# Kernel tuning notes

Measured on AMD Instinct MI355X. Metric: run time of the kernel, lower is better.

## Reference

```python
import jax, jax.numpy as jnp
import numpy as np

HEAD_DIM = 128
ROPE_THETA = 500000.0  # Llama3
NEG_INF = -1e9


def _apply_rope(t, cos, sin):
    # t: [b, s, h, d]; cos/sin: [s, d//2]
    b, s, h, d = t.shape
    tr = t.reshape(b, s, h, d // 2, 2)
    xr, xi = tr[..., 0], tr[..., 1]
    c = cos[None, :, None, :]
    sn = sin[None, :, None, :]
    out = jnp.stack([xr * c - xi * sn, xr * sn + xi * c], axis=-1)
    return out.reshape(b, s, h, d)


def setup_inputs() -> dict:
    key = jax.random.key(0)
    ks = jax.random.split(key, 8)
    bsz, seqlen, model_dim = 2, 2048, 4096
    n_heads, n_kv_heads, head_dim = 32, 8, HEAD_DIM
    max_bsz, max_seqlen = 2, 4096
    pos = 0

    x = jax.random.normal(ks[0], (bsz, seqlen, model_dim), dtype=jnp.float32)
    wq = jax.random.normal(ks[1], (model_dim, n_heads * head_dim), dtype=jnp.float32) * 0.02
    wk = jax.random.normal(ks[2], (model_dim, n_kv_heads * head_dim), dtype=jnp.float32) * 0.02
    wv = jax.random.normal(ks[3], (model_dim, n_kv_heads * head_dim), dtype=jnp.float32) * 0.02
    wo = jax.random.normal(ks[4], (n_heads * head_dim, model_dim), dtype=jnp.float32) * 0.02

    # RoPE tables for positions [pos, pos+seqlen)
    inv_freq = 1.0 / (ROPE_THETA ** (jnp.arange(0, head_dim, 2, dtype=jnp.float32) / head_dim))
    t = jnp.arange(pos, pos + seqlen, dtype=jnp.float32)
    ang = jnp.outer(t, inv_freq)  # [s, d//2]
    freqs_cos, freqs_sin = jnp.cos(ang), jnp.sin(ang)

    # causal additive mask over cached length (pos + seqlen)
    q_idx = jnp.arange(seqlen)[:, None] + pos
    k_idx = jnp.arange(pos + seqlen)[None, :]
    mask = jnp.where(k_idx <= q_idx, 0.0, NEG_INF).astype(jnp.float32)

    k_cache = jnp.zeros((max_bsz, max_seqlen, n_kv_heads, head_dim), dtype=jnp.float32)
    v_cache = jnp.zeros((max_bsz, max_seqlen, n_kv_heads, head_dim), dtype=jnp.float32)
    return {"x": x, "pos": pos, "freqs_cos": freqs_cos, "freqs_sin": freqs_sin,
            "mask": mask, "wq": wq, "wk": wk, "wv": wv, "wo": wo,
            "k_cache": k_cache, "v_cache": v_cache}


def reference(x, pos, freqs_cos, freqs_sin, mask, wq, wk, wv, wo, k_cache, v_cache):
    bsz, seqlen, _ = x.shape
    head_dim = 2 * freqs_cos.shape[-1]
    n_heads = wq.shape[1] // head_dim
    n_kv_heads = wk.shape[1] // head_dim

    q = (x @ wq).reshape(bsz, seqlen, n_heads, head_dim)
    k = (x @ wk).reshape(bsz, seqlen, n_kv_heads, head_dim)
    v = (x @ wv).reshape(bsz, seqlen, n_kv_heads, head_dim)

    q = _apply_rope(q, freqs_cos, freqs_sin)
    k = _apply_rope(k, freqs_cos, freqs_sin)

    # KV-cache append then read back [:, :pos+seqlen]
    k_cache = k_cache.at[:bsz, pos:pos + seqlen].set(k)
    v_cache = v_cache.at[:bsz, pos:pos + seqlen].set(v)
    keys = k_cache[:bsz, :pos + seqlen]      # [b, kv_len, n_kv, d]
    values = v_cache[:bsz, :pos + seqlen]

    repeats = n_heads // n_kv_heads
    keys = jnp.repeat(keys, repeats, axis=2)     # [b, kv_len, h, d]
    values = jnp.repeat(values, repeats, axis=2)

    scale = 1.0 / jnp.sqrt(jnp.float32(head_dim))
    scores = jnp.einsum('bqhd,bkhd->bhqk', q, keys) * scale + mask
    attn = jax.nn.softmax(scores, axis=-1)
    out = jnp.einsum('bhqk,bkhd->bqhd', attn, values)
    out = out.reshape(bsz, seqlen, n_heads * head_dim)
    return out @ wo
```

## Files before the change

kernel.cpp:

```cpp
#include <hip/hip_runtime.h>
#include <hip/hip_bf16.h>

typedef __bf16 bf16x8 __attribute__((ext_vector_type(8)));
typedef float  f32x4  __attribute__((ext_vector_type(4)));

#define DEVI __device__ __forceinline__

DEVI void async_copy16(const void* g, void* s) {
  __builtin_amdgcn_global_load_lds(
      (__attribute__((address_space(1))) void*)g,
      (__attribute__((address_space(3))) void*)s,
      16, 0, 0);
}

DEVI unsigned pack_bf16x2(float lo, float hi) {
  union { __hip_bfloat16 h[2]; unsigned u; } pk;
  pk.h[0] = __float2bfloat16(lo);
  pk.h[1] = __float2bfloat16(hi);
  return pk.u;
}

__global__ __launch_bounds__(256) void cvt_f32_bf16(const float* __restrict__ in,
                                                    __hip_bfloat16* __restrict__ out,
                                                    int n) {
  int i = (blockIdx.x * 256 + threadIdx.x) * 4;
  if (i >= n) return;
  float4 v = *(const float4*)(in + i);
  union { __hip_bfloat16 h[4]; ushort4 u; } o;
  o.h[0] = __float2bfloat16(v.x);
  o.h[1] = __float2bfloat16(v.y);
  o.h[2] = __float2bfloat16(v.z);
  o.h[3] = __float2bfloat16(v.w);
  *(ushort4*)(out + i) = o.u;
}

__global__ __launch_bounds__(256) void transpose_cvt(const float* __restrict__ W,
                                                     __hip_bfloat16* __restrict__ WT,
                                                     int Kdim, int Ndim) {
  __shared__ float tile[32][33];
  int bx = blockIdx.x * 32;
  int by = blockIdx.y * 32;
  int tx = threadIdx.x;
  int ty = threadIdx.y;
  #pragma unroll
  for (int j = 0; j < 32; j += 8)
    tile[ty + j][tx] = W[(size_t)(by + ty + j) * Ndim + bx + tx];
  __syncthreads();
  #pragma unroll
  for (int j = 0; j < 32; j += 8)
    WT[(size_t)(bx + ty + j) * Kdim + by + tx] = __float2bfloat16(tile[tx][ty + j]);
}

__global__ __launch_bounds__(256) void transpose_v(const __hip_bfloat16* __restrict__ vb,
                                                   __hip_bfloat16* __restrict__ vt) {
  __shared__ __hip_bfloat16 tile[32][33];
  const int s0 = blockIdx.x * 32, d0 = blockIdx.y * 32;
  const int bk = blockIdx.z;
  const int bb = bk >> 3, kvh = bk & 7;
  const int tx = threadIdx.x, ty = threadIdx.y;
  #pragma unroll
  for (int j = 0; j < 32; j += 8)
    tile[ty + j][tx] =
        vb[((size_t)(bb * 2048 + s0 + ty + j) * 8 + kvh) * 128 + d0 + tx];
  __syncthreads();
  #pragma unroll
  for (int j = 0; j < 32; j += 8)
    vt[((size_t)bk * 128 + d0 + ty + j) * 2048 + s0 + tx] = tile[tx][ty + j];
}

template <int EPI>
__global__ __launch_bounds__(256) void gemm_bt(
    const __hip_bfloat16* __restrict__ A,
    const __hip_bfloat16* __restrict__ BT,
    float* __restrict__ Cf,
    __hip_bfloat16* __restrict__ Cb,
    __hip_bfloat16* __restrict__ Cb2,
    int M, int N, int K,
    const float* __restrict__ fcos,
    const float* __restrict__ fsin,
    float scale) {
  __shared__ alignas(16) __hip_bfloat16 lds[2][8192];
  const int tid = threadIdx.x;
  const int w = tid >> 6, l = tid & 63;
  const int l4 = l >> 4, l15 = l & 15;
  const int wr = w >> 1, wc = w & 1;
  const int rowBase = blockIdx.y * 128;
  const int colBase = blockIdx.x * 128;

  const __hip_bfloat16* aSrc[2];
  const __hip_bfloat16* bSrc[2];
  int dstOff[2];
  #pragma unroll
  for (int i = 0; i < 2; i++) {
    int c = i * 256 + tid;
    int r = c >> 2;
    int kb = (c & 3) ^ ((r >> 1) & 3);
    aSrc[i] = A  + (size_t)(rowBase + r) * K + kb * 8;
    bSrc[i] = BT + (size_t)(colBase + r) * K + kb * 8;
    dstOff[i] = (i * 256 + w * 64) * 16;
  }

  f32x4 acc[4][4];
  #pragma unroll
  for (int mi = 0; mi < 4; mi++)
    #pragma unroll
    for (int ni = 0; ni < 4; ni++)
      acc[mi][ni] = (f32x4){0.f, 0.f, 0.f, 0.f};

  #pragma unroll
  for (int i = 0; i < 2; i++) {
    async_copy16(aSrc[i], (char*)lds + dstOff[i]);
    async_copy16(bSrc[i], (char*)lds + 8192 + dstOff[i]);
  }

  int cur = 0;
  for (int k0 = 0; k0 < K; k0 += 32) {
    __syncthreads();
    if (k0 + 32 < K) {
      #pragma unroll
      for (int i = 0; i < 2; i++) {
        async_copy16(aSrc[i] + k0 + 32, (char*)lds + (cur ^ 1) * 16384 + dstOff[i]);
        async_copy16(bSrc[i] + k0 + 32, (char*)lds + (cur ^ 1) * 16384 + 8192 + dstOff[i]);
      }
    }
    const char* base = (const char*)lds + cur * 16384;

    bf16x8 aF[4], bF[4];
    #pragma unroll
    for (int mi = 0; mi < 4; mi++) {
      int row = wr * 64 + mi * 16 + l15;
      int phys = l4 ^ ((row >> 1) & 3);
      aF[mi] = *(const bf16x8*)(base + row * 64 + phys * 16);
    }
    #pragma unroll
    for (int ni = 0; ni < 4; ni++) {
      int row = wc * 64 + ni * 16 + l15;
      int phys = l4 ^ ((row >> 1) & 3);
      bF[ni] = *(const bf16x8*)(base + 8192 + row * 64 + phys * 16);
    }
    #pragma unroll
    for (int mi = 0; mi < 4; mi++)
      #pragma unroll
      for (int ni = 0; ni < 4; ni++)
        acc[mi][ni] = __builtin_amdgcn_mfma_f32_16x16x32_bf16(aF[mi], bF[ni], acc[mi][ni], 0, 0, 0);
    cur ^= 1;
  }

  const int orow0 = rowBase + wr * 64 + l4 * 4;
  const int ocol0 = colBase + wc * 64 + l15;
  #pragma unroll
  for (int mi = 0; mi < 4; mi++) {
    #pragma unroll
    for (int ni = 0; ni < 4; ni++) {
      #pragma unroll
      for (int reg = 0; reg < 4; reg++) {
        int r = orow0 + mi * 16 + reg;
        int col = ocol0 + ni * 16;
        float v = acc[mi][ni][reg];
        if constexpr (EPI == 0) {
          Cf[(size_t)r * N + col] = v;
        } else if constexpr (EPI == 1) {
          Cb[(size_t)r * N + col] = __float2bfloat16(v * scale);
        } else if constexpr (EPI == 2) {
          float p = __shfl_xor(v, 1);
          int dd = col & 127;
          int fi = dd >> 1;
          int srow = r & 2047;
          float c = fcos[srow * 64 + fi];
          float s = fsin[srow * 64 + fi];
          float outv = ((col & 1) == 0) ? (v * c - p * s) : (p * s + v * c);
          Cb[(size_t)r * N + col] = __float2bfloat16(outv * scale);
        } else {
          if (colBase < 1024) {
            float p = __shfl_xor(v, 1);
            int dd = col & 127;
            int fi = dd >> 1;
            int srow = r & 2047;
            float c = fcos[srow * 64 + fi];
            float s = fsin[srow * 64 + fi];
            float outv = ((col & 1) == 0) ? (v * c - p * s) : (p * s + v * c);
            Cb[(size_t)r * 1024 + col] = __float2bfloat16(outv);
          } else {
            Cb2[(size_t)r * 1024 + (col - 1024)] = __float2bfloat16(v);
          }
        }
      }
    }
  }
}

__global__ __launch_bounds__(256, 2) void attn_kernel(
    const __hip_bfloat16* __restrict__ Q,
    const __hip_bfloat16* __restrict__ Kb,
    const __hip_bfloat16* __restrict__ Vt_g,
    __hip_bfloat16* __restrict__ O) {
  const int S = 2048, HD = 4096, KVD = 1024, D = 128;
  const int h = blockIdx.y, b = blockIdx.z;
  const int kvh = h >> 2;
  const int bk = b * 8 + kvh;
  const int tid = threadIdx.x;
  const int w = tid >> 6, l = tid & 63;
  const int l4 = l >> 4, l15 = l & 15;

  __shared__ alignas(16) __hip_bfloat16 Kt[2][64 * 128];
  __shared__ alignas(16) __hip_bfloat16 Vt[2][128 * 64];
  __shared__ alignas(16) __hip_bfloat16 Pb[4 * 32 * 64];

  const __hip_bfloat16* kSrc[4];
  const __hip_bfloat16* vSrc[4];
  int stDst[4];
  #pragma unroll
  for (int i = 0; i < 4; i++) {
    int c = i * 256 + tid;
    int kr = c >> 4;
    int kds = (c & 15) ^ (kr & 7);
    kSrc[i] = Kb + (size_t)(b * S + kr) * KVD + kvh * D + kds * 8;
    int vr = c >> 3;
    int vds = (c & 7) ^ (vr & 7);
    vSrc[i] = Vt_g + ((size_t)bk * 128 + vr) * 2048 + vds * 8;
    stDst[i] = (i * 256 + w * 64) * 16;
  }

  char* pbase = (char*)Pb + w * 4096;

  for (int pass = 0; pass < 2; pass++) {
    const int qt = pass ? (15 - blockIdx.x) : blockIdx.x;
    const int qbase = qt * 128 + w * 32;
    const int nt = 2 * qt + 2;

    bf16x8 qf[2][4];
    #pragma unroll
    for (int f = 0; f < 2; f++) {
      const int qrow = qbase + f * 16 + l15;
      const __hip_bfloat16* qptr = Q + (size_t)(b * S + qrow) * HD + h * D + l4 * 8;
      #pragma unroll
      for (int dc = 0; dc < 4; dc++) qf[f][dc] = *(const bf16x8*)(qptr + dc * 32);
    }

    f32x4 o[2][8];
    #pragma unroll
    for (int f = 0; f < 2; f++)
      #pragma unroll
      for (int nf = 0; nf < 8; nf++) o[f][nf] = (f32x4){0.f, 0.f, 0.f, 0.f};
    float mrun[2]  = {-1e30f, -1e30f};
    float llrun[2] = {0.f, 0.f};

    if (pass) __syncthreads();

    #pragma unroll
    for (int i = 0; i < 4; i++) {
      async_copy16(kSrc[i], (char*)Kt + stDst[i]);
      async_copy16(vSrc[i], (char*)Vt + stDst[i]);
    }

    int cur = 0;
    for (int t = 0; t < nt; t++) {
      __syncthreads();
      if (t + 1 < nt) {
        const int kv1 = (t + 1) * 64;
        #pragma unroll
        for (int i = 0; i < 4; i++) {
          async_copy16(kSrc[i] + (size_t)kv1 * KVD, (char*)Kt + (cur ^ 1) * 16384 + stDst[i]);
          async_copy16(vSrc[i] + kv1,               (char*)Vt + (cur ^ 1) * 16384 + stDst[i]);
        }
      }
      const char* ktb = (const char*)Kt + cur * 16384;
      const char* vtb = (const char*)Vt + cur * 16384;
      const int kv0 = t * 64;

      f32x4 s[2][4];
      #pragma unroll
      for (int f = 0; f < 2; f++)
        #pragma unroll
        for (int kg = 0; kg < 4; kg++) s[f][kg] = (f32x4){0.f, 0.f, 0.f, 0.f};
      __builtin_amdgcn_s_setprio(1);
      #pragma unroll
      for (int dc = 0; dc < 4; dc++) {
        #pragma unroll
        for (int kg = 0; kg < 4; kg++) {
          int key = kg * 16 + l15;
          int phys = (dc * 4 + l4) ^ (key & 7);
          bf16x8 kf = *(const bf16x8*)(ktb + key * 256 + phys * 16);
          s[0][kg] = __builtin_amdgcn_mfma_f32_16x16x32_bf16(kf, qf[0][dc], s[0][kg], 0, 0, 0);
          s[1][kg] = __builtin_amdgcn_mfma_f32_16x16x32_bf16(kf, qf[1][dc], s[1][kg], 0, 0, 0);
        }
      }
      __builtin_amdgcn_s_setprio(0);

      if (t >= nt - 2) {
        #pragma unroll
        for (int f = 0; f < 2; f++) {
          int q = qbase + f * 16 + l15;
          #pragma unroll
          for (int kg = 0; kg < 4; kg++)
            #pragma unroll
            for (int reg = 0; reg < 4; reg++)
              if (kv0 + kg * 16 + 4 * l4 + reg > q) s[f][kg][reg] = -1e30f;
        }
      }

      #pragma unroll
      for (int f = 0; f < 2; f++) {
        float pmax = -1e30f;
        #pragma unroll
        for (int kg = 0; kg < 4; kg++)
          #pragma unroll
          for (int reg = 0; reg < 4; reg++) pmax = fmaxf(pmax, s[f][kg][reg]);
        pmax = fmaxf(pmax, __shfl_xor(pmax, 16));
        pmax = fmaxf(pmax, __shfl_xor(pmax, 32));
        float mn = fmaxf(mrun[f], pmax);
        float alpha = __expf(mrun[f] - mn);
        mrun[f] = mn;
        float rs = 0.f;
        #pragma unroll
        for (int kg = 0; kg < 4; kg++)
          #pragma unroll
          for (int reg = 0; reg < 4; reg++) {
            float p = __expf(s[f][kg][reg] - mn);
            s[f][kg][reg] = p;
            rs += p;
          }
        rs += __shfl_xor(rs, 16);
        rs += __shfl_xor(rs, 32);
        llrun[f] = llrun[f] * alpha + rs;

        #pragma unroll
        for (int kg = 0; kg < 4; kg++)
          #pragma unroll
          for (int p2 = 0; p2 < 2; p2++) {
            unsigned u = pack_bf16x2(s[f][kg][2 * p2], s[f][kg][2 * p2 + 1]);
            int slot16 = 2 * kg + (l4 >> 1);
            int inner = (8 * l4 + 4 * p2) & 15;
            *(unsigned*)(pbase + (f * 16 + l15) * 128 + ((slot16 ^ (l15 & 7)) * 16) + inner) = u;
          }

        float alpha_r[4];
        #pragma unroll
        for (int reg = 0; reg < 4; reg++)
          alpha_r[reg] = __shfl(alpha, (l & 48) + 4 * l4 + reg);
        #pragma unroll
        for (int nf = 0; nf < 8; nf++)
          #pragma unroll
          for (int reg = 0; reg < 4; reg++) o[f][nf][reg] *= alpha_r[reg];
      }

      __builtin_amdgcn_s_setprio(1);
      #pragma unroll
      for (int half = 0; half < 2; half++) {
        int physp = (half * 4 + l4) ^ (l15 & 7);
        bf16x8 pa0 = *(const bf16x8*)(pbase + (0 * 16 + l15) * 128 + physp * 16);
        bf16x8 pa1 = *(const bf16x8*)(pbase + (1 * 16 + l15) * 128 + physp * 16);
        #pragma unroll
        for (int nf = 0; nf < 8; nf++) {
          int d = nf * 16 + l15;
          bf16x8 vf = *(const bf16x8*)(vtb + d * 128 + physp * 16);
          o[0][nf] = __builtin_amdgcn_mfma_f32_16x16x32_bf16(pa0, vf, o[0][nf], 0, 0, 0);
          o[1][nf] = __builtin_amdgcn_mfma_f32_16x16x32_bf16(pa1, vf, o[1][nf], 0, 0, 0);
        }
      }
      __builtin_amdgcn_s_setprio(0);
      cur ^= 1;
    }

    #pragma unroll
    for (int f = 0; f < 2; f++) {
      #pragma unroll
      for (int reg = 0; reg < 4; reg++) {
        float llr = __shfl(llrun[f], (l & 48) + 4 * l4 + reg);
        float inv = 1.0f / llr;
        int r = qbase + f * 16 + 4 * l4 + reg;
        __hip_bfloat16* optr = O + (size_t)(b * S + r) * HD + h * D + l15;
        #pragma unroll
        for (int nf = 0; nf < 8; nf++) optr[nf * 16] = __float2bfloat16(o[f][nf][reg] * inv);
      }
    }
  }
}

extern "C" void kernel_launch(void* const* d_in, const int* in_sizes, int n_in,
                              void* d_out, int out_size, void* d_ws, size_t ws_size,
                              hipStream_t stream) {
  const float* x    = (const float*)d_in[0];
  const float* fcos = (const float*)d_in[2];
  const float* fsin = (const float*)d_in[3];
  const float* wq   = (const float*)d_in[5];
  const float* wk   = (const float*)d_in[6];
  const float* wv   = (const float*)d_in[7];
  const float* wo   = (const float*)d_in[8];
  float* out = (float*)d_out;

  char* ws = (char*)d_ws;
  const size_t MB = 1024 * 1024;
  __hip_bfloat16* xb  = (__hip_bfloat16*)(ws + 0);
  __hip_bfloat16* wT  = (__hip_bfloat16*)(ws + 32 * MB);
  __hip_bfloat16* wkT = (__hip_bfloat16*)(ws + 64 * MB);
  __hip_bfloat16* wvT = (__hip_bfloat16*)(ws + 72 * MB);
  __hip_bfloat16* qb  = (__hip_bfloat16*)(ws + 80 * MB);
  __hip_bfloat16* kb  = (__hip_bfloat16*)(ws + 112 * MB);
  __hip_bfloat16* vb  = (__hip_bfloat16*)(ws + 120 * MB);
  __hip_bfloat16* ab  = xb;
  __hip_bfloat16* vt  = wT;

  const float qscale = 0.08838834764831845f;

  cvt_f32_bf16<<<16384, 256, 0, stream>>>(x, xb, 16777216);
  transpose_cvt<<<dim3(128, 128), dim3(32, 8), 0, stream>>>(wq, wT, 4096, 4096);
  transpose_cvt<<<dim3(32, 128), dim3(32, 8), 0, stream>>>(wk, wkT, 4096, 1024);
  transpose_cvt<<<dim3(32, 128), dim3(32, 8), 0, stream>>>(wv, wvT, 4096, 1024);

  gemm_bt<2><<<dim3(32, 32), 256, 0, stream>>>(xb, wT,  nullptr, qb, nullptr,
                                               4096, 4096, 4096, fcos, fsin, qscale);
  gemm_bt<3><<<dim3(16, 32), 256, 0, stream>>>(xb, wkT, nullptr, kb, vb,
                                               4096, 2048, 4096, fcos, fsin, 1.0f);

  transpose_v<<<dim3(64, 4, 16), dim3(32, 8), 0, stream>>>(vb, vt);

  attn_kernel<<<dim3(8, 32, 2), 256, 0, stream>>>(qb, kb, vt, ab);

  transpose_cvt<<<dim3(128, 128), dim3(32, 8), 0, stream>>>(wo, wT, 4096, 4096);
  gemm_bt<0><<<dim3(32, 32), 256, 0, stream>>>(ab, wT, out, nullptr, nullptr,
                                               4096, 4096, 4096, nullptr, nullptr, 1.0f);
}
```

Measured before the change: 579.1 us.

## Deepen GEMM prefetch pipeline and remap blocks for XCD-aware L2 locality

The GEMM kernel now prefetches two k-tiles ahead, using explicit vmcnt/lgkmcnt waits and raw barriers instead of a single __syncthreads per iteration. The next load is issued only after the LDS fragments are read, which overlaps global loads with MFMA, and MFMA runs at raised wave priority. The grid is flattened to 1D and blocks are swizzled so consecutive blocks on each of the 8 XCDs cover neighbouring tiles, aiming for better L2 reuse. The hand-placed waitcnt counts depend on each thread issuing exactly four async copies per stage, and any mismatch would break correctness.

```diff
diff --git a/kernel.cpp b/kernel.cpp
--- a/kernel.cpp
+++ b/kernel.cpp
@@ -75,6 +75,7 @@
     float* __restrict__ Cf,
     __hip_bfloat16* __restrict__ Cb,
     __hip_bfloat16* __restrict__ Cb2,
+    int nx,
     int M, int N, int K,
     const float* __restrict__ fcos,
     const float* __restrict__ fsin,
@@ -84,8 +85,12 @@
   const int w = tid >> 6, l = tid & 63;
   const int l4 = l >> 4, l15 = l & 15;
   const int wr = w >> 1, wc = w & 1;
-  const int rowBase = blockIdx.y * 128;
-  const int colBase = blockIdx.x * 128;
+
+  const int lin = blockIdx.x;
+  const int q = gridDim.x >> 3;
+  const int swz = (lin & 7) * q + (lin >> 3);
+  const int rowBase = (swz / nx) * 128;
+  const int colBase = (swz % nx) * 128;
 
   const __hip_bfloat16* aSrc[2];
   const __hip_bfloat16* bSrc[2];
@@ -112,19 +117,23 @@
     async_copy16(aSrc[i], (char*)lds + dstOff[i]);
     async_copy16(bSrc[i], (char*)lds + 8192 + dstOff[i]);
   }
+  #pragma unroll
+  for (int i = 0; i < 2; i++) {
+    async_copy16(aSrc[i] + 32, (char*)lds + 16384 + dstOff[i]);
+    async_copy16(bSrc[i] + 32, (char*)lds + 16384 + 8192 + dstOff[i]);
+  }
 
   int cur = 0;
   for (int k0 = 0; k0 < K; k0 += 32) {
-    __syncthreads();
     if (k0 + 32 < K) {
-      #pragma unroll
-      for (int i = 0; i < 2; i++) {
-        async_copy16(aSrc[i] + k0 + 32, (char*)lds + (cur ^ 1) * 16384 + dstOff[i]);
-        async_copy16(bSrc[i] + k0 + 32, (char*)lds + (cur ^ 1) * 16384 + 8192 + dstOff[i]);
-      }
-    }
+      asm volatile("s_waitcnt vmcnt(4)" ::: "memory");
+    } else {
+      asm volatile("s_waitcnt vmcnt(0)" ::: "memory");
+    }
+    __builtin_amdgcn_s_barrier();
+    __builtin_amdgcn_sched_barrier(0);
+
     const char* base = (const char*)lds + cur * 16384;
-
     bf16x8 aF[4], bF[4];
     #pragma unroll
     for (int mi = 0; mi < 4; mi++) {
@@ -138,11 +147,26 @@
       int phys = l4 ^ ((row >> 1) & 3);
       bF[ni] = *(const bf16x8*)(base + 8192 + row * 64 + phys * 16);
     }
+    asm volatile("s_waitcnt lgkmcnt(0)" ::: "memory");
+    __builtin_amdgcn_sched_barrier(0);
+    __builtin_amdgcn_s_barrier();
+    __builtin_amdgcn_sched_barrier(0);
+
+    if (k0 + 64 < K) {
+      #pragma unroll
+      for (int i = 0; i < 2; i++) {
+        async_copy16(aSrc[i] + k0 + 64, (char*)lds + cur * 16384 + dstOff[i]);
+        async_copy16(bSrc[i] + k0 + 64, (char*)lds + cur * 16384 + 8192 + dstOff[i]);
+      }
+    }
+
+    __builtin_amdgcn_s_setprio(1);
     #pragma unroll
     for (int mi = 0; mi < 4; mi++)
       #pragma unroll
       for (int ni = 0; ni < 4; ni++)
         acc[mi][ni] = __builtin_amdgcn_mfma_f32_16x16x32_bf16(aF[mi], bF[ni], acc[mi][ni], 0, 0, 0);
+    __builtin_amdgcn_s_setprio(0);
     cur ^= 1;
   }
 
@@ -408,16 +432,16 @@
   transpose_cvt<<<dim3(32, 128), dim3(32, 8), 0, stream>>>(wk, wkT, 4096, 1024);
   transpose_cvt<<<dim3(32, 128), dim3(32, 8), 0, stream>>>(wv, wvT, 4096, 1024);
 
-  gemm_bt<2><<<dim3(32, 32), 256, 0, stream>>>(xb, wT,  nullptr, qb, nullptr,
-                                               4096, 4096, 4096, fcos, fsin, qscale);
-  gemm_bt<3><<<dim3(16, 32), 256, 0, stream>>>(xb, wkT, nullptr, kb, vb,
-                                               4096, 2048, 4096, fcos, fsin, 1.0f);
+  gemm_bt<2><<<1024, 256, 0, stream>>>(xb, wT,  nullptr, qb, nullptr,
+                                       32, 4096, 4096, 4096, fcos, fsin, qscale);
+  gemm_bt<3><<<512, 256, 0, stream>>>(xb, wkT, nullptr, kb, vb,
+                                      16, 4096, 2048, 4096, fcos, fsin, 1.0f);
 
   transpose_v<<<dim3(64, 4, 16), dim3(32, 8), 0, stream>>>(vb, vt);
 
   attn_kernel<<<dim3(8, 32, 2), 256, 0, stream>>>(qb, kb, vt, ab);
 
   transpose_cvt<<<dim3(128, 128), dim3(32, 8), 0, stream>>>(wo, wT, 4096, 4096);
-  gemm_bt<0><<<dim3(32, 32), 256, 0, stream>>>(ab, wT, out, nullptr, nullptr,
-                                               4096, 4096, 4096, nullptr, nullptr, 1.0f);
-}
+  gemm_bt<0><<<1024, 256, 0, stream>>>(ab, wT, out, nullptr, nullptr,
+                                       32, 4096, 4096, 4096, nullptr, nullptr, 1.0f);
+}
```

After: 616.9 us. 1.07x slower.
